# Kernel optimization log

Hardware: AMD Instinct MI355X
Metric: run time of the kernel (lower is better)

Reference implementation:

```python
import jax, jax.numpy as jnp
import numpy as np

# Fixed graph/model dims (see shape_source)
C = 16      # cardinality
SUB = 64    # representation_size // cardinality
R = 1024    # representation_size
E = 1024    # node_encoding_size
S = 1024    # processed spatial feature size
G = 256     # global (FPN) channels
NH = 64     # number of human nodes
N = 256     # total number of nodes (humans first)
P = NH * N  # number of (human, node) pairs
EPS = 1e-5


def _layernorm(x, g, b):
    mu = jnp.mean(x, axis=-1, keepdims=True)
    var = jnp.var(x, axis=-1, keepdims=True)
    return (x - mu) * jax.lax.rsqrt(var + EPS) * g + b


def _pair_head(app, spat, W1, b1, W2, b2, W3, b3):
    # app: [P_or_1, A], spat: [P, S] -> [P, R]  (sum over cardinality; NO outer relu)
    a1 = jnp.einsum('pi,cis->cps', app, W1) + b1[:, None, :]   # [C,P_or_1,SUB]
    a2 = jnp.einsum('pj,cjs->cps', spat, W2) + b2[:, None, :]  # [C,P,SUB]
    h = jax.nn.relu(a1 * a2)                                   # broadcast over P
    return jnp.einsum('cps,csr->pr', h, W3) + jnp.sum(b3, axis=0)


def reference(node_encodings, spatial_raw, global_feat,
              sp_W1, sp_b1, sp_W2, sp_b2, sp_W3, sp_b3,
              ah_W1, ah_b1, ah_W2, ah_b2, ah_W3, ah_b3,
              o2s_W1, o2s_b1, o2s_W2, o2s_b2, o2s_W3, o2s_b3,
              s2o_W1, s2o_b1, s2o_W2, s2o_b2, s2o_W3, s2o_b3,
              ahg_W1, ahg_b1, ahg_W2, ahg_b2, ahg_W3, ahg_b3,
              adj_W, adj_b, lnh_g, lnh_b, lno_g, lno_b):
    # spatial head MLP: 36 -> 128 -> 256 -> 1024 with ReLU
    sp = jax.nn.relu(spatial_raw @ sp_W1 + sp_b1)
    sp = jax.nn.relu(sp @ sp_W2 + sp_b2)
    sp = jax.nn.relu(sp @ sp_W3 + sp_b3)            # [P, S]
    sp3 = sp.reshape(NH, N, S)                      # [NH, N, S]

    x_idx = jnp.repeat(jnp.arange(NH), N)           # [P]
    y_idx = jnp.tile(jnp.arange(N), NH)             # [P]

    h_enc = node_encodings[:NH]                     # humans are permuted to the top
    o_enc = node_encodings

    for _ in range(1):  # num_iter
        app_pairs = jnp.concatenate([h_enc[x_idx], o_enc[y_idx]], axis=1)  # [P, 2E]
        weights = jax.nn.relu(_pair_head(app_pairs, sp, ah_W1, ah_b1, ah_W2, ah_b2, ah_W3, ah_b3))
        adj = (weights @ adj_W + adj_b).reshape(NH, N)

        # obj_to_sub (node_type='object'): appearance = all node encodings
        a1 = jnp.einsum('ni,cis->cns', o_enc, o2s_W1) + o2s_b1[:, None, :]          # [C,N,SUB]
        a2 = jnp.einsum('hnj,cjs->chns', sp3, o2s_W2) + o2s_b2[:, None, None, :]    # [C,NH,N,SUB]
        m = jnp.einsum('chns,csr->hnr', jax.nn.relu(a1[:, None] * a2), o2s_W3) + jnp.sum(o2s_b3, axis=0)
        msg_h = jax.nn.relu(jnp.sum(jax.nn.softmax(adj, axis=1)[..., None] * m, axis=1))  # [NH,R]
        h_enc = _layernorm(h_enc + msg_h, lnh_g, lnh_b)

        # sub_to_obj (node_type='human'): appearance = human encodings
        a1 = jnp.einsum('hi,cis->chs', h_enc, s2o_W1) + s2o_b1[:, None, :]          # [C,NH,SUB]
        a2 = jnp.einsum('hnj,cjs->cnhs', sp3, s2o_W2) + s2o_b2[:, None, None, :]    # [C,N,NH,SUB]
        m = jnp.einsum('cnhs,csr->nhr', jax.nn.relu(a1[:, None] * a2), s2o_W3) + jnp.sum(s2o_b3, axis=0)
        msg_o = jax.nn.relu(jnp.sum(jax.nn.softmax(adj.T, axis=1)[..., None] * m, axis=1))  # [N,R]
        o_enc = _layernorm(o_enc + msg_o, lno_g, lno_b)

    app_final = jnp.concatenate([h_enc[x_idx], o_enc[y_idx]], axis=1)               # [P, 2E]
    f_local = jax.nn.relu(_pair_head(app_final, sp, ah_W1, ah_b1, ah_W2, ah_b2, ah_W3, ah_b3))
    f_glob = jax.nn.relu(_pair_head(global_feat, sp, ahg_W1, ahg_b1, ahg_W2, ahg_b2, ahg_W3, ahg_b3))
    return jnp.concatenate([f_local, f_glob], axis=1)  # [P, 2R]


def setup_inputs() -> dict:
    key = jax.random.key(0)
    ks = iter(jax.random.split(key, 64))
    def rn(shape, scale=0.05):
        return jax.random.normal(next(ks), shape, dtype=jnp.float32) * scale
    inp = {
        'node_encodings': jax.random.normal(next(ks), (N, E), dtype=jnp.float32),
        'spatial_raw': jax.random.normal(next(ks), (P, 36), dtype=jnp.float32),
        'global_feat': jax.random.normal(next(ks), (1, G), dtype=jnp.float32),
        'sp_W1': rn((36, 128)), 'sp_b1': jnp.zeros(128, jnp.float32),
        'sp_W2': rn((128, 256)), 'sp_b2': jnp.zeros(256, jnp.float32),
        'sp_W3': rn((256, S)), 'sp_b3': jnp.zeros(S, jnp.float32),
        'ah_W1': rn((C, 2 * E, SUB)), 'ah_b1': jnp.zeros((C, SUB), jnp.float32),
        'ah_W2': rn((C, S, SUB)), 'ah_b2': jnp.zeros((C, SUB), jnp.float32),
        'ah_W3': rn((C, SUB, R)), 'ah_b3': jnp.zeros((C, R), jnp.float32),
        'o2s_W1': rn((C, E, SUB)), 'o2s_b1': jnp.zeros((C, SUB), jnp.float32),
        'o2s_W2': rn((C, S, SUB)), 'o2s_b2': jnp.zeros((C, SUB), jnp.float32),
        'o2s_W3': rn((C, SUB, R)), 'o2s_b3': jnp.zeros((C, R), jnp.float32),
        's2o_W1': rn((C, E, SUB)), 's2o_b1': jnp.zeros((C, SUB), jnp.float32),
        's2o_W2': rn((C, S, SUB)), 's2o_b2': jnp.zeros((C, SUB), jnp.float32),
        's2o_W3': rn((C, SUB, R)), 's2o_b3': jnp.zeros((C, R), jnp.float32),
        'ahg_W1': rn((C, G, SUB)), 'ahg_b1': jnp.zeros((C, SUB), jnp.float32),
        'ahg_W2': rn((C, S, SUB)), 'ahg_b2': jnp.zeros((C, SUB), jnp.float32),
        'ahg_W3': rn((C, SUB, R)), 'ahg_b3': jnp.zeros((C, R), jnp.float32),
        'adj_W': rn((R, 1)), 'adj_b': jnp.zeros(1, jnp.float32),
        'lnh_g': jnp.ones(E, jnp.float32), 'lnh_b': jnp.zeros(E, jnp.float32),
        'lno_g': jnp.ones(E, jnp.float32), 'lno_b': jnp.zeros(E, jnp.float32),
    }
    return inp
```

## Files before the change

kernel.cpp:

```cpp
#include <hip/hip_runtime.h>
#include <hip/hip_bf16.h>
#include <stdint.h>
#include <stddef.h>

using bf16 = __hip_bfloat16;
typedef __bf16 bf16x8 __attribute__((ext_vector_type(8)));
typedef float f32x4 __attribute__((ext_vector_type(4)));

#define P_  16384

__device__ __forceinline__ void gload16(const void* g, void* l) {
    __builtin_amdgcn_global_load_lds((const __attribute__((address_space(1))) void*)g,
                                     (__attribute__((address_space(3))) void*)l, 16, 0, 0);
}

struct GArgs {
    const bf16* A; const bf16* B; void* C;
    const float* bias;
    const float* aux1;
    const float* aux2;
    int M, N, K, ldc, kchunk, aux_ld;
    void* C2; void* C3;
    const float* b2a; const float* b2b; const float* b2c;
    const float* b1o;  const float* a1gv;
};

template<int MODE, bool RELU, bool BIAS>
__global__ __launch_bounds__(256, 3)
void gemm_bt(GArgs g)
{
    __shared__ __align__(16) bf16 As[128 * 32];
    __shared__ __align__(16) bf16 Bs[128 * 32];

    const int tid  = threadIdx.x;
    const int wave = tid >> 6;
    const int lane = tid & 63;
    const int tileM = blockIdx.x * 128;
    const int tileN = blockIdx.y * 128;
    const int wr = (wave >> 1) << 6;
    const int wc = (wave & 1) << 6;
    const int M = g.M, N = g.N, K = g.K;

    f32x4 acc[4][4] = {};

    int arow[2], brow[2], ako[2];
    #pragma unroll
    for (int j = 0; j < 2; ++j) {
        int c  = wave * 128 + j * 64 + lane;
        int r  = c >> 2;
        ako[j] = (c & 3) << 3;
        int gr = tileM + r; if (gr > M - 1) gr = M - 1;
        arow[j] = gr;
        int gn = tileN + r; if (gn > N - 1) gn = N - 1;
        brow[j] = gn;
    }
    const int m0   = wr + (lane & 15);
    const int n0   = wc + (lane & 15);
    const int koff = (lane >> 4) << 3;

    int kbeg = 0, kend = K;
    if constexpr (MODE == 2) { kbeg = blockIdx.z * g.kchunk; kend = kbeg + g.kchunk; }

    for (int k0 = kbeg; k0 < kend; k0 += 32) {
        #pragma unroll
        for (int j = 0; j < 2; ++j) {
            int c = wave * 128 + j * 64 + lane;
            gload16(g.A + (size_t)arow[j] * K + k0 + ako[j], (void*)(As + c * 8));
            gload16(g.B + (size_t)brow[j] * K + k0 + ako[j], (void*)(Bs + c * 8));
        }
        __syncthreads();
        bf16x8 af[4], bfv[4];
        #pragma unroll
        for (int i = 0; i < 4; ++i) {
            af[i]  = *(const bf16x8*)(As + (m0 + i * 16) * 32 + koff);
            bfv[i] = *(const bf16x8*)(Bs + (n0 + i * 16) * 32 + koff);
        }
        #pragma unroll
        for (int i = 0; i < 4; ++i)
            #pragma unroll
            for (int j = 0; j < 4; ++j)
                acc[i][j] = __builtin_amdgcn_mfma_f32_16x16x32_bf16(af[i], bfv[j], acc[i][j], 0, 0, 0);
        __syncthreads();
    }

    const int rbase = tileM + wr + ((lane >> 4) << 2);
    const int cbase = tileN + wc + (lane & 15);

    if constexpr (MODE == 0 || MODE == 1) {
        #pragma unroll
        for (int i = 0; i < 4; ++i)
            #pragma unroll
            for (int j = 0; j < 4; ++j)
                #pragma unroll
                for (int r = 0; r < 4; ++r) {
                    int grow = rbase + i * 16 + r;
                    if (grow >= M) continue;
                    int gcol = cbase + j * 16;
                    float v = acc[i][j][r];
                    if (BIAS) v += g.bias[gcol];
                    if (RELU) v = fmaxf(v, 0.f);
                    if (MODE == 1) ((bf16*)g.C)[(size_t)grow * g.ldc + gcol] = __float2bfloat16(v);
                    else           ((float*)g.C)[(size_t)grow * g.ldc + gcol] = v;
                }
    } else if constexpr (MODE == 2) {
        #pragma unroll
        for (int i = 0; i < 4; ++i)
            #pragma unroll
            for (int j = 0; j < 4; ++j)
                #pragma unroll
                for (int r = 0; r < 4; ++r) {
                    int grow = rbase + i * 16 + r;
                    if (grow >= M) continue;
                    atomicAdd((float*)g.C + (size_t)grow * g.ldc + cbase + j * 16, acc[i][j][r]);
                }
    } else if constexpr (MODE == 4) {
        #pragma unroll
        for (int i = 0; i < 4; ++i)
            #pragma unroll
            for (int j = 0; j < 4; ++j)
                #pragma unroll
                for (int r = 0; r < 4; ++r) {
                    int p    = rbase + i * 16 + r;
                    int gcol = cbase + j * 16;
                    float a2v = acc[i][j][r] + g.bias[gcol];
                    float a1v = g.aux1[(size_t)(p >> 8) * g.aux_ld + gcol] + g.aux2[gcol];
                    float h = fmaxf(a1v * a2v, 0.f);
                    size_t orow = (size_t)((p & 255) * 64 + (p >> 8));
                    ((bf16*)g.C)[orow * 1024 + gcol] = __float2bfloat16(h);
                }
    } else if constexpr (MODE == 6) {
        #pragma unroll
        for (int i = 0; i < 4; ++i)
            #pragma unroll
            for (int r = 0; r < 4; ++r) {
                float s = 0.f;
                #pragma unroll
                for (int j = 0; j < 4; ++j) {
                    int gcol = cbase + j * 16;
                    s += fmaxf(acc[i][j][r] + g.bias[gcol], 0.f) * g.aux1[gcol];
                }
                s += __shfl_xor(s, 1); s += __shfl_xor(s, 2);
                s += __shfl_xor(s, 4); s += __shfl_xor(s, 8);
                if ((lane & 15) == 0)
                    atomicAdd((float*)g.C + rbase + i * 16 + r, s);
            }
    } else if constexpr (MODE == 7 || MODE == 8) {
        float s[4] = {0.f, 0.f, 0.f, 0.f};
        #pragma unroll
        for (int i = 0; i < 4; ++i)
            #pragma unroll
            for (int r = 0; r < 4; ++r) {
                float wv = g.aux1[rbase + i * 16 + r];
                #pragma unroll
                for (int j = 0; j < 4; ++j) s[j] += wv * acc[i][j][r];
            }
        #pragma unroll
        for (int j = 0; j < 4; ++j) {
            s[j] += __shfl_xor(s[j], 16);
            s[j] += __shfl_xor(s[j], 32);
        }
        if (lane < 16) {
            int outrow = (tileM + wr) >> (MODE == 7 ? 8 : 6);
            #pragma unroll
            for (int j = 0; j < 4; ++j)
                atomicAdd((float*)g.C + (size_t)outrow * 1024 + cbase + j * 16, s[j]);
        }
    } else if constexpr (MODE == 9) {
        int grp = tileN >> 10;
        int lcb = (tileN & 1023) + wc + (lane & 15);
        #pragma unroll
        for (int i = 0; i < 4; ++i)
            #pragma unroll
            for (int j = 0; j < 4; ++j)
                #pragma unroll
                for (int r = 0; r < 4; ++r) {
                    int p    = rbase + i * 16 + r;
                    int lcol = lcb + j * 16;
                    float accv = acc[i][j][r];
                    if (grp == 0) {
                        ((bf16*)g.C)[(size_t)p * 1024 + lcol] =
                            __float2bfloat16(accv + g.b2a[lcol]);
                    } else if (grp == 1) {
                        float a2v = accv + g.b2b[lcol];
                        float a1v = g.aux1[(size_t)(p & 255) * g.aux_ld + lcol] + g.b1o[lcol];
                        ((bf16*)g.C2)[(size_t)p * 1024 + lcol] =
                            __float2bfloat16(fmaxf(a1v * a2v, 0.f));
                    } else {
                        float a2v = accv + g.b2c[lcol];
                        ((bf16*)g.C3)[(size_t)p * 1024 + lcol] =
                            __float2bfloat16(fmaxf(g.a1gv[lcol] * a2v, 0.f));
                    }
                }
    }
}

static GArgs mkargs(const bf16* A, const bf16* B, void* C, const float* bias,
                    const float* aux1, const float* aux2,
                    int M, int N, int K, int ldc, int kchunk, int aux_ld)
{
    GArgs g{};
    g.A = A; g.B = B; g.C = C; g.bias = bias; g.aux1 = aux1; g.aux2 = aux2;
    g.M = M; g.N = N; g.K = K; g.ldc = ldc; g.kchunk = kchunk; g.aux_ld = aux_ld;
    return g;
}

__global__ void transp(const float* __restrict__ src, bf16* __restrict__ dst,
                       int rows, int cols, size_t sstride, size_t dstride)
{
    const float* s = src + blockIdx.z * sstride;
    bf16*        d = dst + blockIdx.z * dstride;
    __shared__ float tile[32][33];
    int c0 = blockIdx.x * 32, r0 = blockIdx.y * 32;
    int x = threadIdx.x, y = threadIdx.y;
    for (int yy = y; yy < 32; yy += 8) {
        int r = r0 + yy, c = c0 + x;
        tile[yy][x] = (r < rows && c < cols) ? s[(size_t)r * cols + c] : 0.f;
    }
    __syncthreads();
    for (int yy = y; yy < 32; yy += 8) {
        int c = c0 + yy, r = r0 + x;
        if (c < cols && r < rows) d[(size_t)c * rows + r] = __float2bfloat16(tile[x][yy]);
    }
}

struct T8 { const float* s[8]; bf16* d[8]; size_t ss[8]; };
__global__ void transp64b(T8 t)
{
    int pair = blockIdx.z >> 4, slice = blockIdx.z & 15;
    const float* s = t.s[pair] + slice * t.ss[pair];
    bf16*        d = t.d[pair] + slice * 65536;
    __shared__ float tile[32][33];
    int c0 = blockIdx.x * 32, r0 = blockIdx.y * 32;
    int x = threadIdx.x, y = threadIdx.y;
    for (int yy = y; yy < 32; yy += 8)
        tile[yy][x] = s[(size_t)(r0 + yy) * 64 + c0 + x];
    __syncthreads();
    for (int yy = y; yy < 32; yy += 8)
        d[(size_t)(c0 + yy) * 1024 + r0 + x] = __float2bfloat16(tile[x][yy]);
}

struct T4 { const float* s[4]; bf16* d[4]; };
__global__ void transp1024b(T4 t)
{
    const float* s = t.s[blockIdx.z];
    bf16*        d = t.d[blockIdx.z];
    __shared__ float tile[32][33];
    int c0 = blockIdx.x * 32, r0 = blockIdx.y * 32;
    int x = threadIdx.x, y = threadIdx.y;
    for (int yy = y; yy < 32; yy += 8)
        tile[yy][x] = s[(size_t)(r0 + yy) * 1024 + c0 + x];
    __syncthreads();
    for (int yy = y; yy < 32; yy += 8)
        d[(size_t)(c0 + yy) * 1024 + r0 + x] = __float2bfloat16(tile[x][yy]);
}

__global__ void conv_spw1(const float* __restrict__ src, bf16* __restrict__ dst) {
    int i = blockIdx.x * 256 + threadIdx.x;
    if (i >= 128 * 64) return;
    int k = i & 63, n = i >> 6;
    dst[i] = __float2bfloat16(k < 36 ? src[k * 128 + n] : 0.f);
}

__global__ void pad_spatial(const float* __restrict__ src, bf16* __restrict__ dst) {
    int i = blockIdx.x * 256 + threadIdx.x;
    int k = i & 63, p = i >> 6;
    dst[i] = __float2bfloat16(k < 36 ? src[p * 36 + k] : 0.f);
}

__global__ void cast_f2b(const float* __restrict__ src, bf16* __restrict__ dst, int n) {
    int i = blockIdx.x * 256 + threadIdx.x;
    if (i < n) dst[i] = __float2bfloat16(src[i]);
}

struct S4 { const float* s[4]; float* d[4]; };
__global__ void sumb3b(S4 a) {
    int i = blockIdx.x * 256 + threadIdx.x;
    int pair = i >> 10, r = i & 1023;
    const float* b3 = a.s[pair];
    float s = 0.f;
    #pragma unroll
    for (int c = 0; c < 16; ++c) s += b3[c * 1024 + r];
    a.d[pair][r] = s;
}

__global__ void hbuild(const float* __restrict__ Ah, int ah_ld,
                       const float* __restrict__ Ao, int ao_ld,
                       const float* __restrict__ b1, const bf16* __restrict__ a2,
                       bf16* __restrict__ H)
{
    size_t base = ((size_t)blockIdx.x * 256 + threadIdx.x) * 8;
    int cs = (int)(base & 1023);
    int p  = (int)(base >> 10);
    const float* ph = Ah + (size_t)(p >> 8) * ah_ld + cs;
    const float* po = Ao + (size_t)(p & 255) * ao_ld + cs;
    bf16x8 av = *(const bf16x8*)(a2 + base);
    bf16x8 o;
    #pragma unroll
    for (int j = 0; j < 8; ++j) {
        float a1 = ph[j] + po[j] + b1[cs + j];
        o[j] = (__bf16)fmaxf(a1 * (float)av[j], 0.f);
    }
    *(bf16x8*)(H + base) = o;
}

__global__ void softmax_h(const float* __restrict__ adj, float* __restrict__ sh) {
    int h = blockIdx.x, n = threadIdx.x;
    __shared__ float red[256];
    float v = adj[h * 256 + n];
    red[n] = v; __syncthreads();
    for (int s = 128; s > 0; s >>= 1) { if (n < s) red[n] = fmaxf(red[n], red[n + s]); __syncthreads(); }
    float m = red[0]; __syncthreads();
    float e = expf(v - m);
    red[n] = e; __syncthreads();
    for (int s = 128; s > 0; s >>= 1) { if (n < s) red[n] += red[n + s]; __syncthreads(); }
    sh[h * 256 + n] = e / red[0];
}

__global__ void softmax_o(const float* __restrict__ adj, float* __restrict__ so) {
    int n = blockIdx.x, h = threadIdx.x;
    float v = adj[h * 256 + n];
    float m = v;
    #pragma unroll
    for (int off = 32; off; off >>= 1) m = fmaxf(m, __shfl_xor(m, off));
    float e = expf(v - m);
    float s = e;
    #pragma unroll
    for (int off = 32; off; off >>= 1) s += __shfl_xor(s, off);
    so[n * 64 + h] = e / s;
}

__global__ void ln_k(const float* __restrict__ x, const float* __restrict__ msgraw,
                     const float* __restrict__ sb3,
                     const float* __restrict__ g, const float* __restrict__ bb,
                     bf16* __restrict__ out)
{
    int row = blockIdx.x, t = threadIdx.x;
    const float* xr = x + (size_t)row * 1024;
    const float* mr = msgraw + (size_t)row * 1024;
    float v[4]; float s = 0.f, ss = 0.f;
    #pragma unroll
    for (int j = 0; j < 4; ++j) {
        int i = t + j * 256;
        v[j] = xr[i] + fmaxf(mr[i] + sb3[i], 0.f);
        s += v[j]; ss += v[j] * v[j];
    }
    __shared__ float r1[256], r2[256];
    r1[t] = s; r2[t] = ss; __syncthreads();
    for (int k = 128; k > 0; k >>= 1) { if (t < k) { r1[t] += r1[t + k]; r2[t] += r2[t + k]; } __syncthreads(); }
    float mean = r1[0] * (1.f / 1024.f);
    float var  = r2[0] * (1.f / 1024.f) - mean * mean;
    float inv  = rsqrtf(var + 1e-5f);
    #pragma unroll
    for (int j = 0; j < 4; ++j) {
        int i = t + j * 256;
        out[(size_t)row * 1024 + i] = __float2bfloat16((v[j] - mean) * inv * g[i] + bb[i]);
    }
}

__global__ void a1g_k(const float* __restrict__ gf, const float* __restrict__ W1,
                      const float* __restrict__ b1, float* __restrict__ a1g)
{
    int cs = blockIdx.x * 256 + threadIdx.x;
    int c = cs >> 6, s = cs & 63;
    float acc = b1[cs];
    for (int g = 0; g < 256; ++g) acc += gf[g] * W1[((size_t)c * 256 + g) * 64 + s];
    a1g[cs] = acc;
}

extern "C" void kernel_launch(void* const* d_in, const int* in_sizes, int n_in,
                              void* d_out, int out_size, void* d_ws, size_t ws_size,
                              hipStream_t stream)
{
    const float* node_enc = (const float*)d_in[0];
    const float* spatial  = (const float*)d_in[1];
    const float* gfeat    = (const float*)d_in[2];
    const float* sp_W1 = (const float*)d_in[3];  const float* sp_b1 = (const float*)d_in[4];
    const float* sp_W2 = (const float*)d_in[5];  const float* sp_b2 = (const float*)d_in[6];
    const float* sp_W3 = (const float*)d_in[7];  const float* sp_b3 = (const float*)d_in[8];
    const float* ah_W1 = (const float*)d_in[9];  const float* ah_b1 = (const float*)d_in[10];
    const float* ah_W2 = (const float*)d_in[11]; const float* ah_b2 = (const float*)d_in[12];
    const float* ah_W3 = (const float*)d_in[13]; const float* ah_b3 = (const float*)d_in[14];
    const float* o2s_W1 = (const float*)d_in[15]; const float* o2s_b1 = (const float*)d_in[16];
    const float* o2s_W2 = (const float*)d_in[17]; const float* o2s_b2 = (const float*)d_in[18];
    const float* o2s_W3 = (const float*)d_in[19]; const float* o2s_b3 = (const float*)d_in[20];
    const float* s2o_W1 = (const float*)d_in[21]; const float* s2o_b1 = (const float*)d_in[22];
    const float* s2o_W2 = (const float*)d_in[23]; const float* s2o_b2 = (const float*)d_in[24];
    const float* s2o_W3 = (const float*)d_in[25]; const float* s2o_b3 = (const float*)d_in[26];
    const float* ahg_W1 = (const float*)d_in[27]; const float* ahg_b1 = (const float*)d_in[28];
    const float* ahg_W2 = (const float*)d_in[29]; const float* ahg_b2 = (const float*)d_in[30];
    const float* ahg_W3 = (const float*)d_in[31]; const float* ahg_b3 = (const float*)d_in[32];
    const float* adj_W = (const float*)d_in[33];
    const float* lnh_g = (const float*)d_in[35]; const float* lnh_b = (const float*)d_in[36];
    const float* lno_g = (const float*)d_in[37]; const float* lno_b = (const float*)d_in[38];

    char* w = (char*)d_ws;
    auto alloc = [&](size_t bytes) { char* p = w; w += (bytes + 255) & ~(size_t)255; return p; };
    bf16*  sp      = (bf16*)alloc((size_t)P_ * 1024 * 2);
    bf16*  a2_ah   = (bf16*)alloc((size_t)P_ * 1024 * 2);
    bf16*  Hbuf    = (bf16*)alloc((size_t)P_ * 1024 * 2);
    bf16*  H_o2s   = (bf16*)alloc((size_t)P_ * 1024 * 2);
    bf16*  H_ahg   = (bf16*)alloc((size_t)P_ * 1024 * 2);
    bf16*  spat_pad= (bf16*)alloc((size_t)P_ * 64 * 2);
    bf16*  spL1    = (bf16*)alloc((size_t)P_ * 128 * 2);
    bf16*  spL2    = (bf16*)alloc((size_t)P_ * 256 * 2);
    bf16*  enc_bf  = (bf16*)alloc(256 * 1024 * 2);
    bf16*  henc_bf = (bf16*)alloc(64 * 1024 * 2);
    bf16*  oenc_bf = (bf16*)alloc(256 * 1024 * 2);
    bf16*  spW1t   = (bf16*)alloc(128 * 64 * 2);
    bf16*  spW2t   = (bf16*)alloc(256 * 128 * 2);
    bf16*  spW3t   = (bf16*)alloc(1024 * 256 * 2);
    bf16*  W2cat   = (bf16*)alloc((size_t)3072 * 1024 * 2);
    bf16*  W1catB  = (bf16*)alloc((size_t)2048 * 1024 * 2);
    bf16*  W1catF  = (bf16*)alloc((size_t)2048 * 1024 * 2);
    bf16*  s2oW2t  = (bf16*)alloc(1024 * 1024 * 2);
    bf16*  ahW3t   = (bf16*)alloc(1024 * 1024 * 2);
    bf16*  o2sW3t  = (bf16*)alloc(1024 * 1024 * 2);
    bf16*  s2oW3t  = (bf16*)alloc(1024 * 1024 * 2);
    bf16*  ahgW3t  = (bf16*)alloc(1024 * 1024 * 2);
    float* Ah    = (float*)alloc(64 * 1024 * 4);
    float* Aoa1  = (float*)alloc(256 * 2048 * 4);
    float* A1f   = (float*)alloc(64 * 2048 * 4);
    float* Ao_f  = (float*)alloc(256 * 1024 * 4);
    size_t z1_bytes = (size_t)(64 * 1024 + 256 * 2048 + 64 * 2048 + 256 * 1024) * 4 + 1024;
    float* adjv  = (float*)alloc(P_ * 4);
    float* msgh  = (float*)alloc(64 * 1024 * 4);
    float* msgo  = (float*)alloc(256 * 1024 * 4);
    size_t z2_bytes = (size_t)(P_ + 64 * 1024 + 256 * 1024) * 4 + 1024;
    float* sh    = (float*)alloc(P_ * 4);
    float* so    = (float*)alloc(P_ * 4);
    float* a1g   = (float*)alloc(1024 * 4);
    float* sb3_ah  = (float*)alloc(4096);
    float* sb3_o2s = (float*)alloc(4096);
    float* sb3_s2o = (float*)alloc(4096);
    float* sb3_ahg = (float*)alloc(4096);

    hipMemsetAsync(Ah,   0, z1_bytes, stream);
    hipMemsetAsync(adjv, 0, z2_bytes, stream);

    {
        T8 t;
        t.s[0] = ah_W1;                     t.d[0] = W1catF + (size_t)1024 * 1024; t.ss[0] = (size_t)2048 * 64;
        t.s[1] = ah_W1 + (size_t)1024 * 64; t.d[1] = W1catB;                       t.ss[1] = (size_t)2048 * 64;
        t.s[2] = o2s_W1;                    t.d[2] = W1catB + (size_t)1024 * 1024; t.ss[2] = 65536;
        t.s[3] = s2o_W1;                    t.d[3] = W1catF;                       t.ss[3] = 65536;
        t.s[4] = ah_W2;                     t.d[4] = W2cat;                        t.ss[4] = 65536;
        t.s[5] = o2s_W2;                    t.d[5] = W2cat + (size_t)1024 * 1024;  t.ss[5] = 65536;
        t.s[6] = ahg_W2;                    t.d[6] = W2cat + (size_t)2048 * 1024;  t.ss[6] = 65536;
        t.s[7] = s2o_W2;                    t.d[7] = s2oW2t;                       t.ss[7] = 65536;
        transp64b<<<dim3(2, 32, 128), dim3(32, 8), 0, stream>>>(t);
    }
    {
        T4 t;
        t.s[0] = ah_W3;  t.d[0] = ahW3t;
        t.s[1] = o2s_W3; t.d[1] = o2sW3t;
        t.s[2] = s2o_W3; t.d[2] = s2oW3t;
        t.s[3] = ahg_W3; t.d[3] = ahgW3t;
        transp1024b<<<dim3(32, 32, 4), dim3(32, 8), 0, stream>>>(t);
    }
    dim3 tb(32, 8);
    conv_spw1<<<32, 256, 0, stream>>>(sp_W1, spW1t);
    transp<<<dim3(8, 4, 1),  tb, 0, stream>>>(sp_W2, spW2t, 128, 256, 0, 0);
    transp<<<dim3(32, 8, 1), tb, 0, stream>>>(sp_W3, spW3t, 256, 1024, 0, 0);
    pad_spatial<<<4096, 256, 0, stream>>>(spatial, spat_pad);
    cast_f2b<<<1024, 256, 0, stream>>>(node_enc, enc_bf, 256 * 1024);
    {
        S4 a;
        a.s[0] = ah_b3;  a.d[0] = sb3_ah;
        a.s[1] = o2s_b3; a.d[1] = sb3_o2s;
        a.s[2] = s2o_b3; a.d[2] = sb3_s2o;
        a.s[3] = ahg_b3; a.d[3] = sb3_ahg;
        sumb3b<<<16, 256, 0, stream>>>(a);
    }
    a1g_k<<<4, 256, 0, stream>>>(gfeat, ahg_W1, ahg_b1, a1g);

    gemm_bt<2, false, false><<<dim3(2, 16, 16), 256, 0, stream>>>(
        mkargs(enc_bf, W1catB, Aoa1, nullptr, nullptr, nullptr, 256, 2048, 1024, 2048, 64, 0));
    gemm_bt<2, false, false><<<dim3(1, 8, 16), 256, 0, stream>>>(
        mkargs(enc_bf, W1catF + (size_t)1024 * 1024, Ah, nullptr, nullptr, nullptr, 64, 1024, 1024, 1024, 64, 0));

    gemm_bt<1, true, true><<<dim3(128, 1), 256, 0, stream>>>(
        mkargs(spat_pad, spW1t, spL1, sp_b1, nullptr, nullptr, P_, 128, 64, 128, 0, 0));
    gemm_bt<1, true, true><<<dim3(128, 2), 256, 0, stream>>>(
        mkargs(spL1, spW2t, spL2, sp_b2, nullptr, nullptr, P_, 256, 128, 256, 0, 0));
    gemm_bt<1, true, true><<<dim3(128, 8), 256, 0, stream>>>(
        mkargs(spL2, spW3t, sp, sp_b3, nullptr, nullptr, P_, 1024, 256, 1024, 0, 0));

    {
        GArgs g = mkargs(sp, W2cat, a2_ah, nullptr, Aoa1 + 1024, nullptr, P_, 3072, 1024, 1024, 0, 2048);
        g.C2 = H_o2s; g.C3 = H_ahg;
        g.b2a = ah_b2; g.b2b = o2s_b2; g.b2c = ahg_b2; g.b1o = o2s_b1; g.a1gv = a1g;
        gemm_bt<9, false, false><<<dim3(128, 24), 256, 0, stream>>>(g);
    }

    hbuild<<<8192, 256, 0, stream>>>(Ah, 1024, Aoa1, 2048, ah_b1, a2_ah, Hbuf);
    gemm_bt<6, false, false><<<dim3(128, 8), 256, 0, stream>>>(
        mkargs(Hbuf, ahW3t, adjv, sb3_ah, adj_W, nullptr, P_, 1024, 1024, 1024, 0, 0));
    softmax_h<<<64, 256, 0, stream>>>(adjv, sh);
    softmax_o<<<256, 64, 0, stream>>>(adjv, so);

    gemm_bt<7, false, false><<<dim3(128, 8), 256, 0, stream>>>(
        mkargs(H_o2s, o2sW3t, msgh, nullptr, sh, nullptr, P_, 1024, 1024, 1024, 0, 0));
    ln_k<<<64, 256, 0, stream>>>(node_enc, msgh, sb3_o2s, lnh_g, lnh_b, henc_bf);

    gemm_bt<2, false, false><<<dim3(1, 16, 16), 256, 0, stream>>>(
        mkargs(henc_bf, W1catF, A1f, nullptr, nullptr, nullptr, 64, 2048, 1024, 2048, 64, 0));

    gemm_bt<4, false, false><<<dim3(128, 8), 256, 0, stream>>>(
        mkargs(sp, s2oW2t, H_o2s , s2o_b2, A1f, s2o_b1, P_, 1024, 1024, 1024, 0, 2048));
    gemm_bt<8, false, false><<<dim3(128, 8), 256, 0, stream>>>(
        mkargs(H_o2s, s2oW3t, msgo, nullptr, so, nullptr, P_, 1024, 1024, 1024, 0, 0));
    ln_k<<<256, 256, 0, stream>>>(node_enc, msgo, sb3_s2o, lno_g, lno_b, oenc_bf);

    gemm_bt<2, false, false><<<dim3(2, 8, 16), 256, 0, stream>>>(
        mkargs(oenc_bf, W1catB, Ao_f, nullptr, nullptr, nullptr, 256, 1024, 1024, 1024, 64, 0));
    hbuild<<<8192, 256, 0, stream>>>(A1f + 1024, 2048, Ao_f, 1024, ah_b1, a2_ah, Hbuf);
    gemm_bt<0, true, true><<<dim3(128, 8), 256, 0, stream>>>(
        mkargs(Hbuf, ahW3t, (float*)d_out, sb3_ah, nullptr, nullptr, P_, 1024, 1024, 2048, 0, 0));

    gemm_bt<0, true, true><<<dim3(128, 8), 256, 0, stream>>>(
        mkargs(H_ahg, ahgW3t, (float*)d_out + 1024, sb3_ahg, nullptr, nullptr, P_, 1024, 1024, 2048, 0, 0));

    (void)in_sizes; (void)n_in; (void)out_size; (void)ws_size;
}
```

Before: 809.8 us.

## Reassociate o2s/s2o message aggregation before W3 projection, fuse s2o W2 and hbuild

The o2s and s2o messages are now computed by first taking the softmax-weighted sum of relu(a1*a2) over pairs, then multiplying the reduced [64 or 256, 1024] matrix by W3. This replaces two full P×1024×1024 GEMMs with small GEMMs plus streaming reductions. The s2o W2 projection is folded into the wide concatenated W2 GEMM (N grows to 4096), and the ah H-buffer build is fused into that GEMM's epilogue. Launch bounds move to 4 blocks per SM. In exchange it writes extra P×1024 intermediates, and it may raise register pressure.

```diff
diff --git a/kernel.cpp b/kernel.cpp
--- a/kernel.cpp
+++ b/kernel.cpp
@@ -18,15 +18,14 @@
     const bf16* A; const bf16* B; void* C;
     const float* bias;
     const float* aux1;
-    const float* aux2;
-    int M, N, K, ldc, kchunk, aux_ld;
-    void* C2; void* C3;
-    const float* b2a; const float* b2b; const float* b2c;
-    const float* b1o;  const float* a1gv;
+    int M, N, K, ldc, kchunk;
+    void* dst1; void* dst2; void* dst3; void* dstH;
+    const float* cb0; const float* cb1; const float* cb2; const float* cb3;
+    const float* a1gv; const float* Ahp; const float* Aop; const float* b1p;
 };
 
 template<int MODE, bool RELU, bool BIAS>
-__global__ __launch_bounds__(256, 3)
+__global__ __launch_bounds__(256, 4)
 void gemm_bt(GArgs g)
 {
     __shared__ __align__(16) bf16 As[128 * 32];
@@ -113,21 +112,6 @@
                     if (grow >= M) continue;
                     atomicAdd((float*)g.C + (size_t)grow * g.ldc + cbase + j * 16, acc[i][j][r]);
                 }
-    } else if constexpr (MODE == 4) {
-        #pragma unroll
-        for (int i = 0; i < 4; ++i)
-            #pragma unroll
-            for (int j = 0; j < 4; ++j)
-                #pragma unroll
-                for (int r = 0; r < 4; ++r) {
-                    int p    = rbase + i * 16 + r;
-                    int gcol = cbase + j * 16;
-                    float a2v = acc[i][j][r] + g.bias[gcol];
-                    float a1v = g.aux1[(size_t)(p >> 8) * g.aux_ld + gcol] + g.aux2[gcol];
-                    float h = fmaxf(a1v * a2v, 0.f);
-                    size_t orow = (size_t)((p & 255) * 64 + (p >> 8));
-                    ((bf16*)g.C)[orow * 1024 + gcol] = __float2bfloat16(h);
-                }
     } else if constexpr (MODE == 6) {
         #pragma unroll
         for (int i = 0; i < 4; ++i)
@@ -144,27 +128,6 @@
                 if ((lane & 15) == 0)
                     atomicAdd((float*)g.C + rbase + i * 16 + r, s);
             }
-    } else if constexpr (MODE == 7 || MODE == 8) {
-        float s[4] = {0.f, 0.f, 0.f, 0.f};
-        #pragma unroll
-        for (int i = 0; i < 4; ++i)
-            #pragma unroll
-            for (int r = 0; r < 4; ++r) {
-                float wv = g.aux1[rbase + i * 16 + r];
-                #pragma unroll
-                for (int j = 0; j < 4; ++j) s[j] += wv * acc[i][j][r];
-            }
-        #pragma unroll
-        for (int j = 0; j < 4; ++j) {
-            s[j] += __shfl_xor(s[j], 16);
-            s[j] += __shfl_xor(s[j], 32);
-        }
-        if (lane < 16) {
-            int outrow = (tileM + wr) >> (MODE == 7 ? 8 : 6);
-            #pragma unroll
-            for (int j = 0; j < 4; ++j)
-                atomicAdd((float*)g.C + (size_t)outrow * 1024 + cbase + j * 16, s[j]);
-        }
     } else if constexpr (MODE == 9) {
         int grp = tileN >> 10;
         int lcb = (tileN & 1023) + wc + (lane & 15);
@@ -178,16 +141,21 @@
                     int lcol = lcb + j * 16;
                     float accv = acc[i][j][r];
                     if (grp == 0) {
-                        ((bf16*)g.C)[(size_t)p * 1024 + lcol] =
-                            __float2bfloat16(accv + g.b2a[lcol]);
+                        bf16 a2b = __float2bfloat16(accv + g.cb0[lcol]);
+                        ((bf16*)g.C)[(size_t)p * 1024 + lcol] = a2b;
+                        float a1 = g.Ahp[((size_t)(p >> 8)) * 1024 + lcol]
+                                 + g.Aop[((size_t)(p & 255)) * 2048 + lcol] + g.b1p[lcol];
+                        ((bf16*)g.dstH)[(size_t)p * 1024 + lcol] =
+                            __float2bfloat16(fmaxf(a1 * (float)a2b, 0.f));
                     } else if (grp == 1) {
-                        float a2v = accv + g.b2b[lcol];
-                        float a1v = g.aux1[(size_t)(p & 255) * g.aux_ld + lcol] + g.b1o[lcol];
-                        ((bf16*)g.C2)[(size_t)p * 1024 + lcol] =
-                            __float2bfloat16(fmaxf(a1v * a2v, 0.f));
+                        ((bf16*)g.dst1)[(size_t)p * 1024 + lcol] =
+                            __float2bfloat16(accv + g.cb1[lcol]);
+                    } else if (grp == 2) {
+                        ((bf16*)g.dst2)[(size_t)p * 1024 + lcol] =
+                            __float2bfloat16(accv + g.cb2[lcol]);
                     } else {
-                        float a2v = accv + g.b2c[lcol];
-                        ((bf16*)g.C3)[(size_t)p * 1024 + lcol] =
+                        float a2v = accv + g.cb3[lcol];
+                        ((bf16*)g.dst3)[(size_t)p * 1024 + lcol] =
                             __float2bfloat16(fmaxf(g.a1gv[lcol] * a2v, 0.f));
                     }
                 }
@@ -195,13 +163,88 @@
 }
 
 static GArgs mkargs(const bf16* A, const bf16* B, void* C, const float* bias,
-                    const float* aux1, const float* aux2,
-                    int M, int N, int K, int ldc, int kchunk, int aux_ld)
+                    const float* aux1, int M, int N, int K, int ldc, int kchunk)
 {
     GArgs g{};
-    g.A = A; g.B = B; g.C = C; g.bias = bias; g.aux1 = aux1; g.aux2 = aux2;
-    g.M = M; g.N = N; g.K = K; g.ldc = ldc; g.kchunk = kchunk; g.aux_ld = aux_ld;
+    g.A = A; g.B = B; g.C = C; g.bias = bias; g.aux1 = aux1;
+    g.M = M; g.N = N; g.K = K; g.ldc = ldc; g.kchunk = kchunk;
     return g;
+}
+
+__global__ void reduce_o2s(const bf16* __restrict__ a2, const float* __restrict__ a1,
+                           const float* __restrict__ b1, const float* __restrict__ sh,
+                           bf16* __restrict__ out)
+{
+    int h = blockIdx.y, cq = blockIdx.x;
+    int ng = threadIdx.x >> 5, ct = threadIdx.x & 31;
+    int c = cq * 256 + ct * 8;
+    float b1v[8], accv[8] = {};
+    #pragma unroll
+    for (int j = 0; j < 8; ++j) b1v[j] = b1[c + j];
+    const float* shh = sh + h * 256;
+    for (int n = ng; n < 256; n += 8) {
+        float w = shh[n];
+        bf16x8 a2v = *(const bf16x8*)(a2 + ((size_t)(h * 256 + n) << 10) + c);
+        const float* a1p = a1 + (size_t)n * 2048 + c;
+        #pragma unroll
+        for (int j = 0; j < 8; ++j)
+            accv[j] += w * fmaxf((a1p[j] + b1v[j]) * (float)a2v[j], 0.f);
+    }
+    __shared__ float red[8][264];
+    #pragma unroll
+    for (int j = 0; j < 8; ++j) red[ng][ct * 8 + j] = accv[j];
+    __syncthreads();
+    for (int s = 4; s > 0; s >>= 1) {
+        if (ng < s)
+            #pragma unroll
+            for (int j = 0; j < 8; ++j) red[ng][ct * 8 + j] += red[ng + s][ct * 8 + j];
+        __syncthreads();
+    }
+    if (ng == 0) {
+        bf16x8 o;
+        #pragma unroll
+        for (int j = 0; j < 8; ++j) o[j] = (__bf16)red[0][ct * 8 + j];
+        *(bf16x8*)(out + (size_t)h * 1024 + c) = o;
+    }
+}
+
+__global__ void reduce_s2o(const bf16* __restrict__ a2, const float* __restrict__ a1,
+                           const float* __restrict__ b1, const float* __restrict__ so,
+                           bf16* __restrict__ out)
+{
+    int n = blockIdx.y, cq = blockIdx.x;
+    int hg = threadIdx.x >> 5, ct = threadIdx.x & 31;
+    int c = cq * 256 + ct * 8;
+    float b1v[8], accv[8] = {};
+    #pragma unroll
+    for (int j = 0; j < 8; ++j) b1v[j] = b1[c + j];
+    const float* son = so + n * 64;
+    #pragma unroll
+    for (int hh = 0; hh < 8; ++hh) {
+        int h = hg + hh * 8;
+        float w = son[h];
+        bf16x8 a2v = *(const bf16x8*)(a2 + ((size_t)(h * 256 + n) << 10) + c);
+        const float* a1p = a1 + (size_t)h * 2048 + c;
+        #pragma unroll
+        for (int j = 0; j < 8; ++j)
+            accv[j] += w * fmaxf((a1p[j] + b1v[j]) * (float)a2v[j], 0.f);
+    }
+    __shared__ float red[8][264];
+    #pragma unroll
+    for (int j = 0; j < 8; ++j) red[hg][ct * 8 + j] = accv[j];
+    __syncthreads();
+    for (int s = 4; s > 0; s >>= 1) {
+        if (hg < s)
+            #pragma unroll
+            for (int j = 0; j < 8; ++j) red[hg][ct * 8 + j] += red[hg + s][ct * 8 + j];
+        __syncthreads();
+    }
+    if (hg == 0) {
+        bf16x8 o;
+        #pragma unroll
+        for (int j = 0; j < 8; ++j) o[j] = (__bf16)red[0][ct * 8 + j];
+        *(bf16x8*)(out + (size_t)n * 1024 + c) = o;
+    }
 }
 
 __global__ void transp(const float* __restrict__ src, bf16* __restrict__ dst,
@@ -398,7 +441,8 @@
     bf16*  sp      = (bf16*)alloc((size_t)P_ * 1024 * 2);
     bf16*  a2_ah   = (bf16*)alloc((size_t)P_ * 1024 * 2);
     bf16*  Hbuf    = (bf16*)alloc((size_t)P_ * 1024 * 2);
-    bf16*  H_o2s   = (bf16*)alloc((size_t)P_ * 1024 * 2);
+    bf16*  a2_o2s  = (bf16*)alloc((size_t)P_ * 1024 * 2);
+    bf16*  a2_s2o  = (bf16*)alloc((size_t)P_ * 1024 * 2);
     bf16*  H_ahg   = (bf16*)alloc((size_t)P_ * 1024 * 2);
     bf16*  spat_pad= (bf16*)alloc((size_t)P_ * 64 * 2);
     bf16*  spL1    = (bf16*)alloc((size_t)P_ * 128 * 2);
@@ -406,13 +450,14 @@
     bf16*  enc_bf  = (bf16*)alloc(256 * 1024 * 2);
     bf16*  henc_bf = (bf16*)alloc(64 * 1024 * 2);
     bf16*  oenc_bf = (bf16*)alloc(256 * 1024 * 2);
+    bf16*  HredH   = (bf16*)alloc(64 * 1024 * 2);
+    bf16*  HredO   = (bf16*)alloc(256 * 1024 * 2);
     bf16*  spW1t   = (bf16*)alloc(128 * 64 * 2);
     bf16*  spW2t   = (bf16*)alloc(256 * 128 * 2);
     bf16*  spW3t   = (bf16*)alloc(1024 * 256 * 2);
-    bf16*  W2cat   = (bf16*)alloc((size_t)3072 * 1024 * 2);
+    bf16*  W2cat   = (bf16*)alloc((size_t)4096 * 1024 * 2);
     bf16*  W1catB  = (bf16*)alloc((size_t)2048 * 1024 * 2);
     bf16*  W1catF  = (bf16*)alloc((size_t)2048 * 1024 * 2);
-    bf16*  s2oW2t  = (bf16*)alloc(1024 * 1024 * 2);
     bf16*  ahW3t   = (bf16*)alloc(1024 * 1024 * 2);
     bf16*  o2sW3t  = (bf16*)alloc(1024 * 1024 * 2);
     bf16*  s2oW3t  = (bf16*)alloc(1024 * 1024 * 2);
@@ -445,8 +490,8 @@
         t.s[3] = s2o_W1;                    t.d[3] = W1catF;                       t.ss[3] = 65536;
         t.s[4] = ah_W2;                     t.d[4] = W2cat;                        t.ss[4] = 65536;
         t.s[5] = o2s_W2;                    t.d[5] = W2cat + (size_t)1024 * 1024;  t.ss[5] = 65536;
-        t.s[6] = ahg_W2;                    t.d[6] = W2cat + (size_t)2048 * 1024;  t.ss[6] = 65536;
-        t.s[7] = s2o_W2;                    t.d[7] = s2oW2t;                       t.ss[7] = 65536;
+        t.s[6] = s2o_W2;                    t.d[6] = W2cat + (size_t)2048 * 1024;  t.ss[6] = 65536;
+        t.s[7] = ahg_W2;                    t.d[7] = W2cat + (size_t)3072 * 1024;  t.ss[7] = 65536;
         transp64b<<<dim3(2, 32, 128), dim3(32, 8), 0, stream>>>(t);
     }
     {
@@ -474,51 +519,51 @@
     a1g_k<<<4, 256, 0, stream>>>(gfeat, ahg_W1, ahg_b1, a1g);
 
     gemm_bt<2, false, false><<<dim3(2, 16, 16), 256, 0, stream>>>(
-        mkargs(enc_bf, W1catB, Aoa1, nullptr, nullptr, nullptr, 256, 2048, 1024, 2048, 64, 0));
+        mkargs(enc_bf, W1catB, Aoa1, nullptr, nullptr, 256, 2048, 1024, 2048, 64));
     gemm_bt<2, false, false><<<dim3(1, 8, 16), 256, 0, stream>>>(
-        mkargs(enc_bf, W1catF + (size_t)1024 * 1024, Ah, nullptr, nullptr, nullptr, 64, 1024, 1024, 1024, 64, 0));
+        mkargs(enc_bf, W1catF + (size_t)1024 * 1024, Ah, nullptr, nullptr, 64, 1024, 1024, 1024, 64));
 
     gemm_bt<1, true, true><<<dim3(128, 1), 256, 0, stream>>>(
-        mkargs(spat_pad, spW1t, spL1, sp_b1, nullptr, nullptr, P_, 128, 64, 128, 0, 0));
+        mkargs(spat_pad, spW1t, spL1, sp_b1, nullptr, P_, 128, 64, 128, 0));
     gemm_bt<1, true, true><<<dim3(128, 2), 256, 0, stream>>>(
-        mkargs(spL1, spW2t, spL2, sp_b2, nullptr, nullptr, P_, 256, 128, 256, 0, 0));
+        mkargs(spL1, spW2t, spL2, sp_b2, nullptr, P_, 256, 128, 256, 0));
     gemm_bt<1, true, true><<<dim3(128, 8), 256, 0, stream>>>(
-        mkargs(spL2, spW3t, sp, sp_b3, nullptr, nullptr, P_, 1024, 256, 1024, 0, 0));
+        mkargs(spL2, spW3t, sp, sp_b3, nullptr, P_, 1024, 256, 1024, 0));
 
     {
-        GArgs g = mkargs(sp, W2cat, a2_ah, nullptr, Aoa1 + 1024, nullptr, P_, 3072, 1024, 1024, 0, 2048);
-        g.C2 = H_o2s; g.C3 = H_ahg;
-        g.b2a = ah_b2; g.b2b = o2s_b2; g.b2c = ahg_b2; g.b1o = o2s_b1; g.a1gv = a1g;
-        gemm_bt<9, false, false><<<dim3(128, 24), 256, 0, stream>>>(g);
-    }
-
-    hbuild<<<8192, 256, 0, stream>>>(Ah, 1024, Aoa1, 2048, ah_b1, a2_ah, Hbuf);
+        GArgs g = mkargs(sp, W2cat, a2_ah, nullptr, nullptr, P_, 4096, 1024, 1024, 0);
+        g.dst1 = a2_o2s; g.dst2 = a2_s2o; g.dst3 = H_ahg; g.dstH = Hbuf;
+        g.cb0 = ah_b2; g.cb1 = o2s_b2; g.cb2 = s2o_b2; g.cb3 = ahg_b2;
+        g.a1gv = a1g; g.Ahp = Ah; g.Aop = Aoa1; g.b1p = ah_b1;
+        gemm_bt<9, false, false><<<dim3(128, 32), 256, 0, stream>>>(g);
+    }
+
     gemm_bt<6, false, false><<<dim3(128, 8), 256, 0, stream>>>(
-        mkargs(Hbuf, ahW3t, adjv, sb3_ah, adj_W, nullptr, P_, 1024, 1024, 1024, 0, 0));
+        mkargs(Hbuf, ahW3t, adjv, sb3_ah, adj_W, P_, 1024, 1024, 1024, 0));
     softmax_h<<<64, 256, 0, stream>>>(adjv, sh);
     softmax_o<<<256, 64, 0, stream>>>(adjv, so);
 
-    gemm_bt<7, false, false><<<dim3(128, 8), 256, 0, stream>>>(
-        mkargs(H_o2s, o2sW3t, msgh, nullptr, sh, nullptr, P_, 1024, 1024, 1024, 0, 0));
+    reduce_o2s<<<dim3(4, 64), 256, 0, stream>>>(a2_o2s, Aoa1 + 1024, o2s_b1, sh, HredH);
+    gemm_bt<2, false, false><<<dim3(1, 8, 16), 256, 0, stream>>>(
+        mkargs(HredH, o2sW3t, msgh, nullptr, nullptr, 64, 1024, 1024, 1024, 64));
     ln_k<<<64, 256, 0, stream>>>(node_enc, msgh, sb3_o2s, lnh_g, lnh_b, henc_bf);
 
     gemm_bt<2, false, false><<<dim3(1, 16, 16), 256, 0, stream>>>(
-        mkargs(henc_bf, W1catF, A1f, nullptr, nullptr, nullptr, 64, 2048, 1024, 2048, 64, 0));
-
-    gemm_bt<4, false, false><<<dim3(128, 8), 256, 0, stream>>>(
-        mkargs(sp, s2oW2t, H_o2s , s2o_b2, A1f, s2o_b1, P_, 1024, 1024, 1024, 0, 2048));
-    gemm_bt<8, false, false><<<dim3(128, 8), 256, 0, stream>>>(
-        mkargs(H_o2s, s2oW3t, msgo, nullptr, so, nullptr, P_, 1024, 1024, 1024, 0, 0));
+        mkargs(henc_bf, W1catF, A1f, nullptr, nullptr, 64, 2048, 1024, 2048, 64));
+
+    reduce_s2o<<<dim3(4, 256), 256, 0, stream>>>(a2_s2o, A1f, s2o_b1, so, HredO);
+    gemm_bt<2, false, false><<<dim3(2, 8, 16), 256, 0, stream>>>(
+        mkargs(HredO, s2oW3t, msgo, nullptr, nullptr, 256, 1024, 1024, 1024, 64));
     ln_k<<<256, 256, 0, stream>>>(node_enc, msgo, sb3_s2o, lno_g, lno_b, oenc_bf);
 
     gemm_bt<2, false, false><<<dim3(2, 8, 16), 256, 0, stream>>>(
-        mkargs(oenc_bf, W1catB, Ao_f, nullptr, nullptr, nullptr, 256, 1024, 1024, 1024, 64, 0));
+        mkargs(oenc_bf, W1catB, Ao_f, nullptr, nullptr, 256, 1024, 1024, 1024, 64));
     hbuild<<<8192, 256, 0, stream>>>(A1f + 1024, 2048, Ao_f, 1024, ah_b1, a2_ah, Hbuf);
     gemm_bt<0, true, true><<<dim3(128, 8), 256, 0, stream>>>(
-        mkargs(Hbuf, ahW3t, (float*)d_out, sb3_ah, nullptr, nullptr, P_, 1024, 1024, 2048, 0, 0));
+        mkargs(Hbuf, ahW3t, (float*)d_out, sb3_ah, nullptr, P_, 1024, 1024, 2048, 0));
 
     gemm_bt<0, true, true><<<dim3(128, 8), 256, 0, stream>>>(
-        mkargs(H_ahg, ahgW3t, (float*)d_out + 1024, sb3_ahg, nullptr, nullptr, P_, 1024, 1024, 2048, 0, 0));
+        mkargs(H_ahg, ahgW3t, (float*)d_out + 1024, sb3_ahg, nullptr, P_, 1024, 1024, 2048, 0));
 
     (void)in_sizes; (void)n_in; (void)out_size; (void)ws_size;
 }
```

Result: no change. 802.8 us (-0.9%).
